# Performance work log

Hardware: AMD Instinct MI355X
Metric: run time of the kernel (lower is better)

## Reference

```python
import jax, jax.numpy as jnp
import numpy as np

HEAD_DIM = 64
NUM_HEADS = 32
ROPE_BASE = 10000.0


def _rope_interleaved(x):
    # x: [B, T, H, D]; interleaved RoPE on query, seqlen_offset = 0
    B, T, H, D = x.shape
    inv_freq = 1.0 / (ROPE_BASE ** (jnp.arange(0, D, 2, dtype=jnp.float32) / D))  # [D/2]
    t = jnp.arange(T, dtype=jnp.float32)
    freqs = t[:, None] * inv_freq[None, :]          # [T, D/2]
    cos = jnp.cos(freqs)[None, :, None, :]          # [1, T, 1, D/2]
    sin = jnp.sin(freqs)[None, :, None, :]
    x1 = x[..., 0::2]
    x2 = x[..., 1::2]
    o1 = x1 * cos - x2 * sin
    o2 = x1 * sin + x2 * cos
    out = jnp.stack([o1, o2], axis=-1).reshape(x.shape)  # re-interleave
    return out


def setup_inputs() -> dict:
    key = jax.random.key(0)
    k1, k2, k3, k4, k5 = jax.random.split(key, 5)
    B, T, Dm = 2, 2048, 2048
    H, Dh = NUM_HEADS, HEAD_DIM
    scale = 0.02
    return {
        "hidden_states": jax.random.normal(k1, (B, T, Dm), jnp.float32),
        "shared_k": jax.random.normal(k2, (B, T, H, Dh), jnp.float32),
        "shared_v": jax.random.normal(k3, (B, T, H, Dh), jnp.float32),
        "Wq": jax.random.normal(k4, (Dm, Dm), jnp.float32) * scale,
        "Wo": jax.random.normal(k5, (Dm, Dm), jnp.float32) * scale,
    }


def reference(hidden_states, shared_k, shared_v, Wq, Wo):
    B, T, Dm = hidden_states.shape
    H, Dh = NUM_HEADS, HEAD_DIM
    # q projection (nn.Linear: x @ W.T)
    q = (hidden_states @ Wq.T).reshape(B, T, H, Dh)
    # rotary on q only (seqlen_offset = shared_k_len - q_len = 0)
    q = _rope_interleaved(q)
    # parallel causal attention over shared KV cache (window_size=None)
    scale = 1.0 / jnp.sqrt(jnp.asarray(Dh, jnp.float32))
    scores = jnp.einsum('bqhd,bkhd->bhqk', q, shared_k) * scale
    causal = jnp.tril(jnp.ones((T, T), dtype=bool))
    scores = jnp.where(causal[None, None], scores, -jnp.inf)
    p = jax.nn.softmax(scores, axis=-1)
    o = jnp.einsum('bhqk,bkhd->bqhd', p, shared_v)
    o = o.reshape(B, T, Dm)
    return o @ Wo.T
```

## Files before the change

### kernel.cpp

```cpp
#include <hip/hip_runtime.h>
#include <stdint.h>

typedef short short8 __attribute__((ext_vector_type(8)));
typedef float f32x4 __attribute__((ext_vector_type(4)));
typedef int int2v __attribute__((ext_vector_type(2)));
typedef int int4v __attribute__((ext_vector_type(4)));

#define QSCALE 0.1803368801111137f
#define FREQC 0.4152410118609203f

__device__ __forceinline__ float bf2f(unsigned short u) {
    union { unsigned int i; float f; } x; x.i = ((unsigned int)u) << 16; return x.f;
}
__device__ __forceinline__ unsigned short f2bf(float f) {
    union { float f; unsigned int i; } x; x.f = f;
    unsigned int i = x.i;
    unsigned int r = i + 0x7FFFu + ((i >> 16) & 1u);
    return (unsigned short)(r >> 16);
}
__device__ __forceinline__ int cvtpk_bf16(float lo, float hi) {
    int r;
    asm("v_cvt_pk_bf16_f32 %0, %1, %2" : "=v"(r) : "v"(lo), "v"(hi));
    return r;
}

#define GLDS16(g, l) \
    __builtin_amdgcn_global_load_lds((const __attribute__((address_space(1))) void*)(g), \
                                     (__attribute__((address_space(3))) void*)(l), 16, 0, 0)

#define WAITVM(n) asm volatile("s_waitcnt vmcnt(" #n ")" ::: "memory")

__global__ void cvt_all(const float* __restrict__ hs, const float* __restrict__ k,
                        const float* __restrict__ wq, const float* __restrict__ wo,
                        unsigned short* __restrict__ hs_b, unsigned short* __restrict__ k_b,
                        unsigned short* __restrict__ wq_b, unsigned short* __restrict__ wo_b) {
    int blk = blockIdx.x;
    const float* in; unsigned short* out; int i;
    if (blk < 8192)        { in = hs; out = hs_b; i = blk * 256 + threadIdx.x; }
    else if (blk < 16384)  { in = k;  out = k_b;  i = (blk - 8192) * 256 + threadIdx.x; }
    else if (blk < 20480)  { in = wq; out = wq_b; i = (blk - 16384) * 256 + threadIdx.x; }
    else                   { in = wo; out = wo_b; i = (blk - 20480) * 256 + threadIdx.x; }
    float4 v = ((const float4*)in)[i];
    ushort4 o;
    o.x = f2bf(v.x); o.y = f2bf(v.y); o.z = f2bf(v.z); o.w = f2bf(v.w);
    ((ushort4*)out)[i] = o;
}

__global__ __launch_bounds__(256) void transpose_v(const float* __restrict__ V, unsigned short* __restrict__ Vt) {
    __shared__ float s[64 * 65];
    int t0 = blockIdx.x * 64;
    int bh = blockIdx.y;
    int b = bh >> 5, h = bh & 31;
    int tid = threadIdx.x;
#pragma unroll
    for (int it = 0; it < 4; ++it) {
        int c = tid + it * 256;
        int t = c >> 4;
        int d0 = (c & 15) * 4;
        float4 v = *(const float4*)(V + (size_t)(((b * 2048 + t0 + t) * 32 + h)) * 64 + d0);
        s[t * 65 + d0 + 0] = v.x; s[t * 65 + d0 + 1] = v.y;
        s[t * 65 + d0 + 2] = v.z; s[t * 65 + d0 + 3] = v.w;
    }
    __syncthreads();
#pragma unroll
    for (int it = 0; it < 2; ++it) {
        int c = tid + it * 256;
        int d = c >> 3;
        int tt = (c & 7) * 8;
        short8 pk;
#pragma unroll
        for (int j = 0; j < 8; ++j) pk[j] = (short)f2bf(s[(tt + j) * 65 + d]);
        *(short8*)(Vt + (size_t)(bh * 64 + d) * 2048 + t0 + tt) = pk;
    }
}

template <bool BF16_OUT>
__global__ __launch_bounds__(256) void gemm_bt(
    const unsigned short* __restrict__ A,
    const unsigned short* __restrict__ B,
    void* __restrict__ Cout,
    int M, int N, int K)
{
    __shared__ __align__(16) unsigned short lA[2][128 * 64];
    __shared__ __align__(16) unsigned short lB[2][128 * 64];
    int tid = threadIdx.x, lane = tid & 63, wave = tid >> 6;
    int wm = (wave >> 1) * 64, wn = (wave & 1) * 64;
    int m16 = lane & 15, q = lane >> 4;
    int rowBase = blockIdx.x * 128, colBase = blockIdx.y * 128;
    f32x4 acc[4][4] = {};

    int sr = lane >> 3;
    int g  = (lane & 7) ^ sr;
    const unsigned short* gAp = A + (size_t)(rowBase + wave * 32 + sr) * K + g * 8;
    const unsigned short* gBp = B + (size_t)(colBase + wave * 32 + sr) * K + g * 8;

#define GSTAGE(buf, k0)                                                                      \
    do {                                                                                     \
        _Pragma("unroll")                                                                    \
        for (int gi = 0; gi < 4; ++gi) {                                                     \
            GLDS16(gAp + (size_t)(8 * gi) * K + (k0), &lA[buf][(wave * 32 + 8 * gi) * 64]);  \
            GLDS16(gBp + (size_t)(8 * gi) * K + (k0), &lB[buf][(wave * 32 + 8 * gi) * 64]);  \
        }                                                                                    \
    } while (0)

    GSTAGE(0, 0);
    WAITVM(0);
    __builtin_amdgcn_s_barrier();
    int cur = 0;
    for (int k0 = 0; k0 < K; k0 += 64) {
        if (k0 + 64 < K) {
            GSTAGE(cur ^ 1, k0 + 64);
            WAITVM(8);
        } else {
            WAITVM(0);
        }
        __builtin_amdgcn_s_barrier();
        const unsigned short* la = lA[cur];
        const unsigned short* lb = lB[cur];
#pragma unroll
        for (int kk = 0; kk < 2; ++kk) {
            short8 af[4], bfr[4];
#pragma unroll
            for (int i2 = 0; i2 < 4; ++i2) {
                int RA = wm + i2 * 16 + m16;
                af[i2]  = *(const short8*)&la[RA * 64 + (((kk * 4 + q) ^ (RA & 7)) * 8)];
                int RB = wn + i2 * 16 + m16;
                bfr[i2] = *(const short8*)&lb[RB * 64 + (((kk * 4 + q) ^ (RB & 7)) * 8)];
            }
#pragma unroll
            for (int i2 = 0; i2 < 4; ++i2)
#pragma unroll
                for (int jn = 0; jn < 4; ++jn)
                    acc[i2][jn] = __builtin_amdgcn_mfma_f32_16x16x32_bf16(af[i2], bfr[jn], acc[i2][jn], 0, 0, 0);
        }
        __builtin_amdgcn_s_barrier();
        cur ^= 1;
    }
#pragma unroll
    for (int i = 0; i < 4; ++i)
#pragma unroll
        for (int jn = 0; jn < 4; ++jn)
#pragma unroll
            for (int r = 0; r < 4; ++r) {
                int row = rowBase + wm + i * 16 + q * 4 + r;
                int col = colBase + wn + jn * 16 + m16;
                float v = acc[i][jn][r];
                if (BF16_OUT) ((unsigned short*)Cout)[(size_t)row * N + col] = f2bf(v);
                else          ((float*)Cout)[(size_t)row * N + col] = v;
            }
}

__global__ __launch_bounds__(256, 3) void attn(
    const unsigned short* __restrict__ Q,
    const unsigned short* __restrict__ Kb,
    const unsigned short* __restrict__ Vt,
    unsigned short* __restrict__ O)
{
    __shared__ __align__(16) unsigned short sK[3][64 * 64];
    __shared__ __align__(16) unsigned short sV[3][64 * 64];
    int tid = threadIdx.x, lane = tid & 63, w = tid >> 6;
    int m16 = lane & 15, q = lane >> 4;
    int rx = m16 & 7;
    int flat = blockIdx.x;
    int bh = flat & 63, p = flat >> 6;
    int b = bh >> 5, h = bh & 31;
    int qtA = 31 - p, qtB = p;

    short8 aqA0, aqA1, aqB0, aqB1;
    {
        int tA = qtA * 64 + w * 16 + m16;
        int tB = qtB * 64 + w * 16 + m16;
        const unsigned short* rowA = Q + (size_t)(b * 2048 + tA) * 2048 + h * 64 + q * 8;
        const unsigned short* rowB = Q + (size_t)(b * 2048 + tB) * 2048 + h * 64 + q * 8;
        short8 a0 = *(const short8*)rowA, a1 = *(const short8*)(rowA + 32);
        short8 b0 = *(const short8*)rowB, b1 = *(const short8*)(rowB + 32);
        float tfA = (float)tA, tfB = (float)tB;
#pragma unroll
        for (int j = 0; j < 4; ++j) {
            float inv0 = __builtin_amdgcn_exp2f(-FREQC * (float)(q * 4 + j));
            float inv1 = __builtin_amdgcn_exp2f(-FREQC * (float)(16 + q * 4 + j));
            float cA0 = __cosf(tfA * inv0), sA0 = __sinf(tfA * inv0);
            float cA1 = __cosf(tfA * inv1), sA1 = __sinf(tfA * inv1);
            float cB0 = __cosf(tfB * inv0), sB0 = __sinf(tfB * inv0);
            float cB1 = __cosf(tfB * inv1), sB1 = __sinf(tfB * inv1);
            float x1, x2;
            x1 = bf2f((unsigned short)a0[2 * j]); x2 = bf2f((unsigned short)a0[2 * j + 1]);
            aqA0[2 * j]     = (short)f2bf((x1 * cA0 - x2 * sA0) * QSCALE);
            aqA0[2 * j + 1] = (short)f2bf((x1 * sA0 + x2 * cA0) * QSCALE);
            x1 = bf2f((unsigned short)a1[2 * j]); x2 = bf2f((unsigned short)a1[2 * j + 1]);
            aqA1[2 * j]     = (short)f2bf((x1 * cA1 - x2 * sA1) * QSCALE);
            aqA1[2 * j + 1] = (short)f2bf((x1 * sA1 + x2 * cA1) * QSCALE);
            x1 = bf2f((unsigned short)b0[2 * j]); x2 = bf2f((unsigned short)b0[2 * j + 1]);
            aqB0[2 * j]     = (short)f2bf((x1 * cB0 - x2 * sB0) * QSCALE);
            aqB0[2 * j + 1] = (short)f2bf((x1 * sB0 + x2 * cB0) * QSCALE);
            x1 = bf2f((unsigned short)b1[2 * j]); x2 = bf2f((unsigned short)b1[2 * j + 1]);
            aqB1[2 * j]     = (short)f2bf((x1 * cB1 - x2 * sB1) * QSCALE);
            aqB1[2 * j + 1] = (short)f2bf((x1 * sB1 + x2 * cB1) * QSCALE);
        }
    }

    float lrunA = 0.f, lrunB = 0.f;
    f32x4 accOA[4], accOB[4];
#pragma unroll
    for (int nt = 0; nt < 4; ++nt) {
        f32x4 z = {0.f, 0.f, 0.f, 0.f};
        accOA[nt] = z; accOB[nt] = z;
    }

    int sr = lane >> 3, g = (lane & 7) ^ sr;
    int rb = w * 16;
    const unsigned short* kgp = Kb + (size_t)(b * 2048 + rb + sr) * 2048 + h * 64 + g * 8;
    const unsigned short* vgp = Vt + (size_t)((b * 32 + h) * 64 + rb + sr) * 2048 + g * 8;

#define ASTAGE(kt, bi)                                                                \
    do {                                                                              \
        int kb0 = (kt) * 64;                                                          \
        _Pragma("unroll")                                                             \
        for (int gi = 0; gi < 2; ++gi) {                                              \
            GLDS16(kgp + (size_t)(kb0 + 8 * gi) * 2048, &sK[bi][(rb + 8 * gi) * 64]); \
            GLDS16(vgp + (size_t)(8 * gi) * 2048 + kb0, &sV[bi][(rb + 8 * gi) * 64]); \
        }                                                                             \
    } while (0)

    ASTAGE(0, 0);
    WAITVM(0);
    __builtin_amdgcn_s_barrier();
    int cur = 0, nxt = 1;
    for (int kt = 0; kt <= qtA; ++kt) {
        if (kt < qtA) {
            ASTAGE(kt + 1, nxt);
            WAITVM(4);
        } else {
            WAITVM(0);
        }
        __builtin_amdgcn_s_barrier();
        bool doB = (kt <= qtB);
        bool diagA = (kt == qtA), diagB = (kt == qtB);
        const unsigned short* kbuf = sK[cur];
        const unsigned short* vbuf = sV[cur];

        int pkA[4][2], pkB[4][2];
#pragma unroll
        for (int nt = 0; nt < 4; ++nt) {
            const unsigned short* kr = kbuf + (nt * 16 + m16) * 64;
            short8 bk0 = *(const short8*)&kr[(q ^ rx) * 8];
            short8 bk1 = *(const short8*)&kr[((4 + q) ^ rx) * 8];
            f32x4 zA = {0.f, 0.f, 0.f, 0.f};
            zA = __builtin_amdgcn_mfma_f32_16x16x32_bf16(bk0, aqA0, zA, 0, 0, 0);
            zA = __builtin_amdgcn_mfma_f32_16x16x32_bf16(bk1, aqA1, zA, 0, 0, 0);
            float e[4];
#pragma unroll
            for (int r = 0; r < 4; ++r) {
                float s = zA[r];
                if (diagA && (nt * 16 + q * 4 + r > w * 16 + m16)) s = -__builtin_inff();
                e[r] = __builtin_amdgcn_exp2f(s);
            }
            lrunA += (e[0] + e[1]) + (e[2] + e[3]);
            pkA[nt][0] = cvtpk_bf16(e[0], e[1]);
            pkA[nt][1] = cvtpk_bf16(e[2], e[3]);
            if (doB) {
                f32x4 zB = {0.f, 0.f, 0.f, 0.f};
                zB = __builtin_amdgcn_mfma_f32_16x16x32_bf16(bk0, aqB0, zB, 0, 0, 0);
                zB = __builtin_amdgcn_mfma_f32_16x16x32_bf16(bk1, aqB1, zB, 0, 0, 0);
                float eb[4];
#pragma unroll
                for (int r = 0; r < 4; ++r) {
                    float s = zB[r];
                    if (diagB && (nt * 16 + q * 4 + r > w * 16 + m16)) s = -__builtin_inff();
                    eb[r] = __builtin_amdgcn_exp2f(s);
                }
                lrunB += (eb[0] + eb[1]) + (eb[2] + eb[3]);
                pkB[nt][0] = cvtpk_bf16(eb[0], eb[1]);
                pkB[nt][1] = cvtpk_bf16(eb[2], eb[3]);
            }
        }

        int4v tA0 = {pkA[0][0], pkA[0][1], pkA[1][0], pkA[1][1]};
        int4v tA1 = {pkA[2][0], pkA[2][1], pkA[3][0], pkA[3][1]};
        short8 apA0 = __builtin_bit_cast(short8, tA0);
        short8 apA1 = __builtin_bit_cast(short8, tA1);
        short8 apB0, apB1;
        if (doB) {
            int4v tB0 = {pkB[0][0], pkB[0][1], pkB[1][0], pkB[1][1]};
            int4v tB1 = {pkB[2][0], pkB[2][1], pkB[3][0], pkB[3][1]};
            apB0 = __builtin_bit_cast(short8, tB0);
            apB1 = __builtin_bit_cast(short8, tB1);
        }

#pragma unroll
        for (int nt = 0; nt < 4; ++nt) {
            const unsigned short* vr = vbuf + (nt * 16 + m16) * 64;
            int2v a0 = *(const int2v*)&vr[(((q >> 1) + 0) ^ rx) * 8 + (q & 1) * 4];
            int2v a1 = *(const int2v*)&vr[(((q >> 1) + 2) ^ rx) * 8 + (q & 1) * 4];
            int2v a2 = *(const int2v*)&vr[(((q >> 1) + 4) ^ rx) * 8 + (q & 1) * 4];
            int2v a3 = *(const int2v*)&vr[(((q >> 1) + 6) ^ rx) * 8 + (q & 1) * 4];
            int4v tv0 = {a0.x, a0.y, a1.x, a1.y};
            int4v tv1 = {a2.x, a2.y, a3.x, a3.y};
            short8 bv0 = __builtin_bit_cast(short8, tv0);
            short8 bv1 = __builtin_bit_cast(short8, tv1);
            accOA[nt] = __builtin_amdgcn_mfma_f32_16x16x32_bf16(apA0, bv0, accOA[nt], 0, 0, 0);
            accOA[nt] = __builtin_amdgcn_mfma_f32_16x16x32_bf16(apA1, bv1, accOA[nt], 0, 0, 0);
            if (doB) {
                accOB[nt] = __builtin_amdgcn_mfma_f32_16x16x32_bf16(apB0, bv0, accOB[nt], 0, 0, 0);
                accOB[nt] = __builtin_amdgcn_mfma_f32_16x16x32_bf16(apB1, bv1, accOB[nt], 0, 0, 0);
            }
        }
        cur = (cur == 2) ? 0 : cur + 1;
        nxt = (nxt == 2) ? 0 : nxt + 1;
    }

    lrunA += __shfl_xor(lrunA, 16); lrunA += __shfl_xor(lrunA, 32);
    lrunB += __shfl_xor(lrunB, 16); lrunB += __shfl_xor(lrunB, 32);
    float invA = 1.0f / lrunA, invB = 1.0f / lrunB;
    float nA[4], nB[4];
#pragma unroll
    for (int r = 0; r < 4; ++r) {
        nA[r] = __shfl(invA, q * 4 + r);
        nB[r] = __shfl(invB, q * 4 + r);
    }
#pragma unroll
    for (int nt = 0; nt < 4; ++nt)
#pragma unroll
        for (int r = 0; r < 4; ++r) {
            int col = h * 64 + nt * 16 + m16;
            O[(size_t)(b * 2048 + qtA * 64 + w * 16 + q * 4 + r) * 2048 + col] =
                f2bf(accOA[nt][r] * nA[r]);
            O[(size_t)(b * 2048 + qtB * 64 + w * 16 + q * 4 + r) * 2048 + col] =
                f2bf(accOB[nt][r] * nB[r]);
        }
}

extern "C" void kernel_launch(void* const* d_in, const int* in_sizes, int n_in,
                              void* d_out, int out_size, void* d_ws, size_t ws_size,
                              hipStream_t stream) {
    const float* hs = (const float*)d_in[0];
    const float* sk = (const float*)d_in[1];
    const float* sv = (const float*)d_in[2];
    const float* wq = (const float*)d_in[3];
    const float* wo = (const float*)d_in[4];
    float* out = (float*)d_out;

    char* ws = (char*)d_ws;
    unsigned short* hid_b = (unsigned short*)(ws);
    unsigned short* wq_b  = (unsigned short*)(ws + ((size_t)16 << 20));
    unsigned short* wo_b  = (unsigned short*)(ws + ((size_t)24 << 20));
    unsigned short* k_b   = (unsigned short*)(ws + ((size_t)32 << 20));
    unsigned short* vt_b  = (unsigned short*)(ws + ((size_t)48 << 20));
    unsigned short* q_b   = (unsigned short*)(ws + ((size_t)64 << 20));
    unsigned short* o_b   = (unsigned short*)(ws + ((size_t)80 << 20));

    cvt_all<<<24576, 256, 0, stream>>>(hs, sk, wq, wo, hid_b, k_b, wq_b, wo_b);
    transpose_v<<<dim3(32, 64), 256, 0, stream>>>(sv, vt_b);
    gemm_bt<true><<<dim3(32, 16), 256, 0, stream>>>(hid_b, wq_b, (void*)q_b, 4096, 2048, 2048);
    attn<<<1024, 256, 0, stream>>>(q_b, k_b, vt_b, o_b);
    gemm_bt<false><<<dim3(32, 16), 256, 0, stream>>>(o_b, wo_b, (void*)out, 4096, 2048, 2048);
}
```

Baseline: 297.5 us.

## Process four query tiles per attention block and merge conversion kernels

Each attention block now handles four causal-balanced query tiles (31-p, 16+p, 15-p, p) instead of two, so every K/V tile loaded into LDS is reused by up to four query tiles, and the grid shrinks to 512 blocks. K/V staging drops from triple to double buffering with an added end-of-iteration barrier, and occupancy hints go from 3 to 2 blocks per CU. The V transpose is folded into the dtype-conversion kernel to save a launch. The cost is higher register pressure and fewer blocks to hide latency, with 512 blocks covering the CUs less evenly.

```diff
diff --git a/kernel.cpp b/kernel.cpp
--- a/kernel.cpp
+++ b/kernel.cpp
@@ -30,28 +30,32 @@
 
 #define WAITVM(n) asm volatile("s_waitcnt vmcnt(" #n ")" ::: "memory")
 
-__global__ void cvt_all(const float* __restrict__ hs, const float* __restrict__ k,
-                        const float* __restrict__ wq, const float* __restrict__ wo,
-                        unsigned short* __restrict__ hs_b, unsigned short* __restrict__ k_b,
-                        unsigned short* __restrict__ wq_b, unsigned short* __restrict__ wo_b) {
+__global__ __launch_bounds__(256) void cvt_tr(
+    const float* __restrict__ hs, const float* __restrict__ k,
+    const float* __restrict__ wq, const float* __restrict__ wo,
+    const float* __restrict__ V,
+    unsigned short* __restrict__ hs_b, unsigned short* __restrict__ k_b,
+    unsigned short* __restrict__ wq_b, unsigned short* __restrict__ wo_b,
+    unsigned short* __restrict__ Vt) {
+    __shared__ float s[64 * 65];
     int blk = blockIdx.x;
-    const float* in; unsigned short* out; int i;
-    if (blk < 8192)        { in = hs; out = hs_b; i = blk * 256 + threadIdx.x; }
-    else if (blk < 16384)  { in = k;  out = k_b;  i = (blk - 8192) * 256 + threadIdx.x; }
-    else if (blk < 20480)  { in = wq; out = wq_b; i = (blk - 16384) * 256 + threadIdx.x; }
-    else                   { in = wo; out = wo_b; i = (blk - 20480) * 256 + threadIdx.x; }
-    float4 v = ((const float4*)in)[i];
-    ushort4 o;
-    o.x = f2bf(v.x); o.y = f2bf(v.y); o.z = f2bf(v.z); o.w = f2bf(v.w);
-    ((ushort4*)out)[i] = o;
-}
-
-__global__ __launch_bounds__(256) void transpose_v(const float* __restrict__ V, unsigned short* __restrict__ Vt) {
-    __shared__ float s[64 * 65];
-    int t0 = blockIdx.x * 64;
-    int bh = blockIdx.y;
+    int tid = threadIdx.x;
+    if (blk < 24576) {
+        const float* in; unsigned short* out; int i;
+        if (blk < 8192)        { in = hs; out = hs_b; i = blk * 256 + tid; }
+        else if (blk < 16384)  { in = k;  out = k_b;  i = (blk - 8192) * 256 + tid; }
+        else if (blk < 20480)  { in = wq; out = wq_b; i = (blk - 16384) * 256 + tid; }
+        else                   { in = wo; out = wo_b; i = (blk - 20480) * 256 + tid; }
+        float4 v = ((const float4*)in)[i];
+        ushort4 o;
+        o.x = f2bf(v.x); o.y = f2bf(v.y); o.z = f2bf(v.z); o.w = f2bf(v.w);
+        ((ushort4*)out)[i] = o;
+        return;
+    }
+    int tb = blk - 24576;
+    int t0 = (tb & 31) * 64;
+    int bh = tb >> 5;
     int b = bh >> 5, h = bh & 31;
-    int tid = threadIdx.x;
 #pragma unroll
     for (int it = 0; it < 4; ++it) {
         int c = tid + it * 256;
@@ -150,61 +154,60 @@
             }
 }
 
-__global__ __launch_bounds__(256, 3) void attn(
+__global__ __launch_bounds__(256, 2) void attn(
     const unsigned short* __restrict__ Q,
     const unsigned short* __restrict__ Kb,
     const unsigned short* __restrict__ Vt,
     unsigned short* __restrict__ O)
 {
-    __shared__ __align__(16) unsigned short sK[3][64 * 64];
-    __shared__ __align__(16) unsigned short sV[3][64 * 64];
+    __shared__ __align__(16) unsigned short sK[2][64 * 64];
+    __shared__ __align__(16) unsigned short sV[2][64 * 64];
     int tid = threadIdx.x, lane = tid & 63, w = tid >> 6;
     int m16 = lane & 15, q = lane >> 4;
     int rx = m16 & 7;
     int flat = blockIdx.x;
     int bh = flat & 63, p = flat >> 6;
     int b = bh >> 5, h = bh & 31;
-    int qtA = 31 - p, qtB = p;
-
-    short8 aqA0, aqA1, aqB0, aqB1;
+    int tA = 31 - p, tB = 16 + p, tC = 15 - p, tD = p;
+
+    short8 aqA0, aqA1, aqB0, aqB1, aqC0, aqC1, aqD0, aqD1;
     {
-        int tA = qtA * 64 + w * 16 + m16;
-        int tB = qtB * 64 + w * 16 + m16;
-        const unsigned short* rowA = Q + (size_t)(b * 2048 + tA) * 2048 + h * 64 + q * 8;
-        const unsigned short* rowB = Q + (size_t)(b * 2048 + tB) * 2048 + h * 64 + q * 8;
-        short8 a0 = *(const short8*)rowA, a1 = *(const short8*)(rowA + 32);
-        short8 b0 = *(const short8*)rowB, b1 = *(const short8*)(rowB + 32);
-        float tfA = (float)tA, tfB = (float)tB;
+        int rA = tA * 64 + w * 16 + m16, rB = tB * 64 + w * 16 + m16;
+        int rC = tC * 64 + w * 16 + m16, rD = tD * 64 + w * 16 + m16;
+        const unsigned short* pA = Q + (size_t)(b * 2048 + rA) * 2048 + h * 64 + q * 8;
+        const unsigned short* pB = Q + (size_t)(b * 2048 + rB) * 2048 + h * 64 + q * 8;
+        const unsigned short* pC = Q + (size_t)(b * 2048 + rC) * 2048 + h * 64 + q * 8;
+        const unsigned short* pD = Q + (size_t)(b * 2048 + rD) * 2048 + h * 64 + q * 8;
+        short8 a0 = *(const short8*)pA, a1 = *(const short8*)(pA + 32);
+        short8 b0 = *(const short8*)pB, b1 = *(const short8*)(pB + 32);
+        short8 c0 = *(const short8*)pC, c1 = *(const short8*)(pC + 32);
+        short8 d0 = *(const short8*)pD, d1 = *(const short8*)(pD + 32);
+        float tfA = (float)rA, tfB = (float)rB, tfC = (float)rC, tfD = (float)rD;
 #pragma unroll
         for (int j = 0; j < 4; ++j) {
             float inv0 = __builtin_amdgcn_exp2f(-FREQC * (float)(q * 4 + j));
             float inv1 = __builtin_amdgcn_exp2f(-FREQC * (float)(16 + q * 4 + j));
-            float cA0 = __cosf(tfA * inv0), sA0 = __sinf(tfA * inv0);
-            float cA1 = __cosf(tfA * inv1), sA1 = __sinf(tfA * inv1);
-            float cB0 = __cosf(tfB * inv0), sB0 = __sinf(tfB * inv0);
-            float cB1 = __cosf(tfB * inv1), sB1 = __sinf(tfB * inv1);
-            float x1, x2;
-            x1 = bf2f((unsigned short)a0[2 * j]); x2 = bf2f((unsigned short)a0[2 * j + 1]);
-            aqA0[2 * j]     = (short)f2bf((x1 * cA0 - x2 * sA0) * QSCALE);
-            aqA0[2 * j + 1] = (short)f2bf((x1 * sA0 + x2 * cA0) * QSCALE);
-            x1 = bf2f((unsigned short)a1[2 * j]); x2 = bf2f((unsigned short)a1[2 * j + 1]);
-            aqA1[2 * j]     = (short)f2bf((x1 * cA1 - x2 * sA1) * QSCALE);
-            aqA1[2 * j + 1] = (short)f2bf((x1 * sA1 + x2 * cA1) * QSCALE);
-            x1 = bf2f((unsigned short)b0[2 * j]); x2 = bf2f((unsigned short)b0[2 * j + 1]);
-            aqB0[2 * j]     = (short)f2bf((x1 * cB0 - x2 * sB0) * QSCALE);
-            aqB0[2 * j + 1] = (short)f2bf((x1 * sB0 + x2 * cB0) * QSCALE);
-            x1 = bf2f((unsigned short)b1[2 * j]); x2 = bf2f((unsigned short)b1[2 * j + 1]);
-            aqB1[2 * j]     = (short)f2bf((x1 * cB1 - x2 * sB1) * QSCALE);
-            aqB1[2 * j + 1] = (short)f2bf((x1 * sB1 + x2 * cB1) * QSCALE);
-        }
-    }
-
-    float lrunA = 0.f, lrunB = 0.f;
-    f32x4 accOA[4], accOB[4];
+            float x1, x2, cc, ss;
+#define ROPE1(dst, src, tf, inv)                                          \
+            cc = __cosf((tf) * (inv)); ss = __sinf((tf) * (inv));         \
+            x1 = bf2f((unsigned short)src[2 * j]);                        \
+            x2 = bf2f((unsigned short)src[2 * j + 1]);                    \
+            dst[2 * j]     = (short)f2bf((x1 * cc - x2 * ss) * QSCALE);   \
+            dst[2 * j + 1] = (short)f2bf((x1 * ss + x2 * cc) * QSCALE)
+            ROPE1(aqA0, a0, tfA, inv0); ROPE1(aqA1, a1, tfA, inv1);
+            ROPE1(aqB0, b0, tfB, inv0); ROPE1(aqB1, b1, tfB, inv1);
+            ROPE1(aqC0, c0, tfC, inv0); ROPE1(aqC1, c1, tfC, inv1);
+            ROPE1(aqD0, d0, tfD, inv0); ROPE1(aqD1, d1, tfD, inv1);
+#undef ROPE1
+        }
+    }
+
+    float lrunA = 0.f, lrunB = 0.f, lrunC = 0.f, lrunD = 0.f;
+    f32x4 accOA[4], accOB[4], accOC[4], accOD[4];
 #pragma unroll
     for (int nt = 0; nt < 4; ++nt) {
         f32x4 z = {0.f, 0.f, 0.f, 0.f};
-        accOA[nt] = z; accOB[nt] = z;
+        accOA[nt] = z; accOB[nt] = z; accOC[nt] = z; accOD[nt] = z;
     }
 
     int sr = lane >> 3, g = (lane & 7) ^ sr;
@@ -225,67 +228,68 @@
     ASTAGE(0, 0);
     WAITVM(0);
     __builtin_amdgcn_s_barrier();
-    int cur = 0, nxt = 1;
-    for (int kt = 0; kt <= qtA; ++kt) {
-        if (kt < qtA) {
-            ASTAGE(kt + 1, nxt);
+    int cur = 0;
+    for (int kt = 0; kt <= tA; ++kt) {
+        if (kt < tA) {
+            ASTAGE(kt + 1, cur ^ 1);
             WAITVM(4);
         } else {
             WAITVM(0);
         }
         __builtin_amdgcn_s_barrier();
-        bool doB = (kt <= qtB);
-        bool diagA = (kt == qtA), diagB = (kt == qtB);
+        bool doB = (kt <= tB), doC = (kt <= tC), doD = (kt <= tD);
+        bool dgA = (kt == tA), dgB = (kt == tB), dgC = (kt == tC), dgD = (kt == tD);
         const unsigned short* kbuf = sK[cur];
         const unsigned short* vbuf = sV[cur];
 
-        int pkA[4][2], pkB[4][2];
+        int pkA[4][2], pkB[4][2], pkC[4][2], pkD[4][2];
 #pragma unroll
         for (int nt = 0; nt < 4; ++nt) {
             const unsigned short* kr = kbuf + (nt * 16 + m16) * 64;
             short8 bk0 = *(const short8*)&kr[(q ^ rx) * 8];
             short8 bk1 = *(const short8*)&kr[((4 + q) ^ rx) * 8];
-            f32x4 zA = {0.f, 0.f, 0.f, 0.f};
-            zA = __builtin_amdgcn_mfma_f32_16x16x32_bf16(bk0, aqA0, zA, 0, 0, 0);
-            zA = __builtin_amdgcn_mfma_f32_16x16x32_bf16(bk1, aqA1, zA, 0, 0, 0);
-            float e[4];
-#pragma unroll
-            for (int r = 0; r < 4; ++r) {
-                float s = zA[r];
-                if (diagA && (nt * 16 + q * 4 + r > w * 16 + m16)) s = -__builtin_inff();
-                e[r] = __builtin_amdgcn_exp2f(s);
-            }
-            lrunA += (e[0] + e[1]) + (e[2] + e[3]);
-            pkA[nt][0] = cvtpk_bf16(e[0], e[1]);
-            pkA[nt][1] = cvtpk_bf16(e[2], e[3]);
-            if (doB) {
-                f32x4 zB = {0.f, 0.f, 0.f, 0.f};
-                zB = __builtin_amdgcn_mfma_f32_16x16x32_bf16(bk0, aqB0, zB, 0, 0, 0);
-                zB = __builtin_amdgcn_mfma_f32_16x16x32_bf16(bk1, aqB1, zB, 0, 0, 0);
-                float eb[4];
-#pragma unroll
-                for (int r = 0; r < 4; ++r) {
-                    float s = zB[r];
-                    if (diagB && (nt * 16 + q * 4 + r > w * 16 + m16)) s = -__builtin_inff();
-                    eb[r] = __builtin_amdgcn_exp2f(s);
-                }
-                lrunB += (eb[0] + eb[1]) + (eb[2] + eb[3]);
-                pkB[nt][0] = cvtpk_bf16(eb[0], eb[1]);
-                pkB[nt][1] = cvtpk_bf16(eb[2], eb[3]);
-            }
-        }
-
-        int4v tA0 = {pkA[0][0], pkA[0][1], pkA[1][0], pkA[1][1]};
-        int4v tA1 = {pkA[2][0], pkA[2][1], pkA[3][0], pkA[3][1]};
-        short8 apA0 = __builtin_bit_cast(short8, tA0);
-        short8 apA1 = __builtin_bit_cast(short8, tA1);
-        short8 apB0, apB1;
-        if (doB) {
-            int4v tB0 = {pkB[0][0], pkB[0][1], pkB[1][0], pkB[1][1]};
-            int4v tB1 = {pkB[2][0], pkB[2][1], pkB[3][0], pkB[3][1]};
-            apB0 = __builtin_bit_cast(short8, tB0);
-            apB1 = __builtin_bit_cast(short8, tB1);
-        }
+#define QKONE(AQ0, AQ1, DG, LRUN, PK)                                                  \
+            do {                                                                       \
+                f32x4 z = {0.f, 0.f, 0.f, 0.f};                                        \
+                z = __builtin_amdgcn_mfma_f32_16x16x32_bf16(bk0, AQ0, z, 0, 0, 0);     \
+                z = __builtin_amdgcn_mfma_f32_16x16x32_bf16(bk1, AQ1, z, 0, 0, 0);     \
+                float e0, e1, e2, e3;                                                  \
+                {                                                                      \
+                    float s0 = z[0], s1 = z[1], s2 = z[2], s3 = z[3];                  \
+                    if (DG) {                                                          \
+                        int qi = w * 16 + m16, kb = nt * 16 + q * 4;                   \
+                        if (kb + 0 > qi) s0 = -__builtin_inff();                       \
+                        if (kb + 1 > qi) s1 = -__builtin_inff();                       \
+                        if (kb + 2 > qi) s2 = -__builtin_inff();                       \
+                        if (kb + 3 > qi) s3 = -__builtin_inff();                       \
+                    }                                                                  \
+                    e0 = __builtin_amdgcn_exp2f(s0); e1 = __builtin_amdgcn_exp2f(s1);  \
+                    e2 = __builtin_amdgcn_exp2f(s2); e3 = __builtin_amdgcn_exp2f(s3);  \
+                }                                                                      \
+                LRUN += (e0 + e1) + (e2 + e3);                                         \
+                PK[nt][0] = cvtpk_bf16(e0, e1);                                        \
+                PK[nt][1] = cvtpk_bf16(e2, e3);                                        \
+            } while (0)
+            QKONE(aqA0, aqA1, dgA, lrunA, pkA);
+            if (doB) QKONE(aqB0, aqB1, dgB, lrunB, pkB);
+            if (doC) QKONE(aqC0, aqC1, dgC, lrunC, pkC);
+            if (doD) QKONE(aqD0, aqD1, dgD, lrunD, pkD);
+#undef QKONE
+        }
+
+#define PACK2(AP0, AP1, PK)                                                     \
+        short8 AP0, AP1;                                                        \
+        {                                                                       \
+            int4v t0 = {PK[0][0], PK[0][1], PK[1][0], PK[1][1]};                \
+            int4v t1 = {PK[2][0], PK[2][1], PK[3][0], PK[3][1]};                \
+            AP0 = __builtin_bit_cast(short8, t0);                               \
+            AP1 = __builtin_bit_cast(short8, t1);                               \
+        }
+        PACK2(apA0, apA1, pkA)
+        PACK2(apB0, apB1, pkB)
+        PACK2(apC0, apC1, pkC)
+        PACK2(apD0, apD1, pkD)
+#undef PACK2
 
 #pragma unroll
         for (int nt = 0; nt < 4; ++nt) {
@@ -304,30 +308,40 @@
                 accOB[nt] = __builtin_amdgcn_mfma_f32_16x16x32_bf16(apB0, bv0, accOB[nt], 0, 0, 0);
                 accOB[nt] = __builtin_amdgcn_mfma_f32_16x16x32_bf16(apB1, bv1, accOB[nt], 0, 0, 0);
             }
-        }
-        cur = (cur == 2) ? 0 : cur + 1;
-        nxt = (nxt == 2) ? 0 : nxt + 1;
-    }
-
-    lrunA += __shfl_xor(lrunA, 16); lrunA += __shfl_xor(lrunA, 32);
-    lrunB += __shfl_xor(lrunB, 16); lrunB += __shfl_xor(lrunB, 32);
-    float invA = 1.0f / lrunA, invB = 1.0f / lrunB;
-    float nA[4], nB[4];
-#pragma unroll
-    for (int r = 0; r < 4; ++r) {
-        nA[r] = __shfl(invA, q * 4 + r);
-        nB[r] = __shfl(invB, q * 4 + r);
-    }
-#pragma unroll
-    for (int nt = 0; nt < 4; ++nt)
-#pragma unroll
-        for (int r = 0; r < 4; ++r) {
-            int col = h * 64 + nt * 16 + m16;
-            O[(size_t)(b * 2048 + qtA * 64 + w * 16 + q * 4 + r) * 2048 + col] =
-                f2bf(accOA[nt][r] * nA[r]);
-            O[(size_t)(b * 2048 + qtB * 64 + w * 16 + q * 4 + r) * 2048 + col] =
-                f2bf(accOB[nt][r] * nB[r]);
-        }
+            if (doC) {
+                accOC[nt] = __builtin_amdgcn_mfma_f32_16x16x32_bf16(apC0, bv0, accOC[nt], 0, 0, 0);
+                accOC[nt] = __builtin_amdgcn_mfma_f32_16x16x32_bf16(apC1, bv1, accOC[nt], 0, 0, 0);
+            }
+            if (doD) {
+                accOD[nt] = __builtin_amdgcn_mfma_f32_16x16x32_bf16(apD0, bv0, accOD[nt], 0, 0, 0);
+                accOD[nt] = __builtin_amdgcn_mfma_f32_16x16x32_bf16(apD1, bv1, accOD[nt], 0, 0, 0);
+            }
+        }
+        __builtin_amdgcn_s_barrier();
+        cur ^= 1;
+    }
+
+#define EPILOG(LRUN, ACC, TQ)                                                              \
+    do {                                                                                   \
+        float l = LRUN;                                                                    \
+        l += __shfl_xor(l, 16); l += __shfl_xor(l, 32);                                    \
+        float inv = 1.0f / l;                                                              \
+        _Pragma("unroll")                                                                  \
+        for (int r = 0; r < 4; ++r) {                                                      \
+            float nv = __shfl(inv, q * 4 + r);                                             \
+            _Pragma("unroll")                                                              \
+            for (int nt = 0; nt < 4; ++nt) {                                               \
+                int col = h * 64 + nt * 16 + m16;                                          \
+                O[(size_t)(b * 2048 + (TQ) * 64 + w * 16 + q * 4 + r) * 2048 + col] =      \
+                    f2bf(ACC[nt][r] * nv);                                                 \
+            }                                                                              \
+        }                                                                                  \
+    } while (0)
+    EPILOG(lrunA, accOA, tA);
+    EPILOG(lrunB, accOB, tB);
+    EPILOG(lrunC, accOC, tC);
+    EPILOG(lrunD, accOD, tD);
+#undef EPILOG
 }
 
 extern "C" void kernel_launch(void* const* d_in, const int* in_sizes, int n_in,
@@ -349,9 +363,8 @@
     unsigned short* q_b   = (unsigned short*)(ws + ((size_t)64 << 20));
     unsigned short* o_b   = (unsigned short*)(ws + ((size_t)80 << 20));
 
-    cvt_all<<<24576, 256, 0, stream>>>(hs, sk, wq, wo, hid_b, k_b, wq_b, wo_b);
-    transpose_v<<<dim3(32, 64), 256, 0, stream>>>(sv, vt_b);
+    cvt_tr<<<26624, 256, 0, stream>>>(hs, sk, wq, wo, sv, hid_b, k_b, wq_b, wo_b, vt_b);
     gemm_bt<true><<<dim3(32, 16), 256, 0, stream>>>(hid_b, wq_b, (void*)q_b, 4096, 2048, 2048);
-    attn<<<1024, 256, 0, stream>>>(q_b, k_b, vt_b, o_b);
+    attn<<<512, 256, 0, stream>>>(q_b, k_b, vt_b, o_b);
     gemm_bt<false><<<dim3(32, 16), 256, 0, stream>>>(o_b, wo_b, (void*)out, 4096, 2048, 2048);
 }
```

Result: no change. 294.1 us (-1.1%).
